# Kernel optimization log

Hardware: AMD Instinct MI355X
Metric: run time of the kernel (lower is better)

## Reference

```python
import jax, jax.numpy as jnp
import numpy as np

V_CNT = 10000
B = 16
N = B * V_CNT          # total nodes
K = 6                  # Chebyshev order
CH = [3, 128, 64, 32, 128]
G = 8                  # GroupNorm groups (divides 128, 64, 32)
EPS = 1e-5
AVG_DEG = 16


def setup_inputs() -> dict:
    key = jax.random.key(0)
    ks = jax.random.split(key, 8)
    n_edges = N * AVG_DEG
    inp = {
        "x": jax.random.normal(ks[0], (N, CH[0]), jnp.float32),
        "edge_index": jax.random.randint(ks[1], (2, n_edges), 0, N, jnp.int32).astype(jnp.int64),
    }
    for l in range(3):
        cin, cout = CH[l], CH[l + 1]
        s = (1.0 / (cin * K)) ** 0.5
        inp[f"W{l}"] = jax.random.uniform(ks[2 + l], (K, cin, cout), jnp.float32, -s, s)
        inp[f"b{l}"] = jnp.zeros((cout,), jnp.float32)
        inp[f"gamma{l}"] = jnp.ones((cout,), jnp.float32)
        inp[f"beta{l}"] = jnp.zeros((cout,), jnp.float32)
    din = V_CNT * CH[3]
    s = (1.0 / din) ** 0.5
    inp["W_last"] = jax.random.uniform(ks[5], (din, CH[4]), jnp.float32, -s, s)
    inp["b_last"] = jnp.zeros((CH[4],), jnp.float32)
    return inp


def _cheb_edge_weights(edge_index):
    # PyG ChebConv sym normalization with lambda_max=2: L_hat = L - I = -D^{-1/2} A D^{-1/2}
    row, col = edge_index[0], edge_index[1]
    deg = jax.ops.segment_sum(jnp.ones(row.shape, jnp.float32), row, num_segments=N)
    dis = jnp.where(deg > 0, jax.lax.rsqrt(jnp.maximum(deg, 1.0)), 0.0)  # deg^{-1/2}, inf->0
    return -dis[row] * dis[col], row, col


def _cheb_conv(x, row, col, w, W, b):
    # Chebyshev recursion: Tx0=x, Tx1=L_hat x, Tx_k = 2 L_hat Tx_{k-1} - Tx_{k-2}
    prop = lambda h: jax.ops.segment_sum(w[:, None] * h[col], row, num_segments=N)
    Tx0 = x
    out = Tx0 @ W[0]
    Tx1 = prop(Tx0)
    out = out + Tx1 @ W[1]
    for k in range(2, W.shape[0]):
        Tx2 = 2.0 * prop(Tx1) - Tx0
        out = out + Tx2 @ W[k]
        Tx0, Tx1 = Tx1, Tx2
    return out + b


def _group_norm(h, gamma, beta):
    n, C = h.shape
    hg = h.reshape(n, G, C // G)
    mu = hg.mean(axis=2, keepdims=True)
    var = hg.var(axis=2, keepdims=True)
    hg = (hg - mu) * jax.lax.rsqrt(var + EPS)
    return hg.reshape(n, C) * gamma + beta


def reference(x, edge_index, W0, b0, gamma0, beta0, W1, b1, gamma1, beta1,
              W2, b2, gamma2, beta2, W_last, b_last):
    w, row, col = _cheb_edge_weights(edge_index)
    Ws = [W0, W1, W2]
    bs = [b0, b1, b2]
    gs = [gamma0, gamma1, gamma2]
    betas = [beta0, beta1, beta2]
    h = x
    for l in range(3):
        h = _cheb_conv(h, row, col, w, Ws[l], bs[l])
        h = _group_norm(h, gs[l], betas[l])
        h = jax.nn.relu(h)
    h = h.reshape(-1, V_CNT * CH[3])  # [B, v_cnt*32]
    return h @ W_last + b_last
```

## Files before the change

### kernel.cpp

```cpp
#include <hip/hip_runtime.h>
#include <hip/hip_fp16.h>


#define NN 160000
#define EE 2560000
#define FDC 640

typedef __attribute__((ext_vector_type(8))) _Float16 half8;
typedef __attribute__((ext_vector_type(4))) float floatx4;

__device__ inline float2 h2f2(unsigned u) {
  __half2 h = __builtin_bit_cast(__half2, u);
  return __half22float2(h);
}
__device__ inline unsigned short f2h(float f) {
  return __builtin_bit_cast(unsigned short, __float2half_rn(f));
}
__device__ inline unsigned packh2(float a, float b) {
  return __builtin_bit_cast(unsigned, __floats2half2_rn(a, b));
}

__global__ __launch_bounds__(256) void k_zero(int* __restrict__ p, int n) {
  int i = blockIdx.x * 256 + threadIdx.x;
  if (i < n) p[i] = 0;
}

__global__ __launch_bounds__(256) void k_hist(const int* __restrict__ ei, int* __restrict__ deg) {
  int e = blockIdx.x * 256 + threadIdx.x;
  if (e < EE) atomicAdd(&deg[ei[e]], 1);
}

__global__ __launch_bounds__(256) void k_dis(const int* __restrict__ deg, float* __restrict__ dis) {
  int i = blockIdx.x * 256 + threadIdx.x;
  if (i < NN) { int d = deg[i]; dis[i] = d > 0 ? rsqrtf((float)d) : 0.f; }
}

__global__ __launch_bounds__(256) void k_scan1(const int* __restrict__ deg, int* __restrict__ rowStart,
                                               int* __restrict__ bsum) {
  __shared__ int s[256];
  int tid = threadIdx.x;
  int i = blockIdx.x * 256 + tid;
  int v = deg[i];
  s[tid] = v;
  __syncthreads();
  for (int off = 1; off < 256; off <<= 1) {
    int t = (tid >= off) ? s[tid - off] : 0;
    __syncthreads();
    s[tid] += t;
    __syncthreads();
  }
  rowStart[i] = s[tid] - v;
  if (tid == 255) bsum[blockIdx.x] = s[255];
}

__global__ void k_scan2(int* __restrict__ bsum, int nb) {
  __shared__ int s[1024];
  int tid = threadIdx.x;
  int v = (tid < nb) ? bsum[tid] : 0;
  s[tid] = v;
  __syncthreads();
  for (int off = 1; off < 1024; off <<= 1) {
    int t = (tid >= off) ? s[tid - off] : 0;
    __syncthreads();
    s[tid] += t;
    __syncthreads();
  }
  if (tid < nb) bsum[tid] = s[tid] - v;
}

__global__ __launch_bounds__(256) void k_scan3(int* __restrict__ rowStart, const int* __restrict__ bsum) {
  int i = blockIdx.x * 256 + threadIdx.x;
  rowStart[i] += bsum[blockIdx.x];
  if (i == 0) rowStart[NN] = EE;
}

__global__ __launch_bounds__(256) void k_scatter(const int* __restrict__ ei, const int* __restrict__ rowStart,
                                                 int* __restrict__ cursor, const float* __restrict__ dis,
                                                 int2* __restrict__ ew) {
  int e = blockIdx.x * 256 + threadIdx.x;
  if (e >= EE) return;
  int r = ei[e];
  int c = ei[EE + e];
  int pos = rowStart[r] + atomicAdd(&cursor[r], 1);
  ew[pos] = make_int2(c, __float_as_int(-dis[r] * dis[c]));
}

__global__ __launch_bounds__(256) void k_copyx(const float* __restrict__ x, float* __restrict__ A,
                                               unsigned short* __restrict__ TxAll) {
  int i = blockIdx.x * 256 + threadIdx.x;
  if (i < NN * 3) {
    float v = x[i];
    A[i] = v;
    int node = i / 3, c = i - node * 3;
    TxAll[node * 32 + c] = f2h(v);
  }
}

template <int MODE>
__global__ __launch_bounds__(256) void k_prop3(const float* __restrict__ Tsrc, float* __restrict__ Tdst,
                                               unsigned short* __restrict__ TxAll, int ks,
                                               const int* __restrict__ rowStart, const int2* __restrict__ ew) {
  int i = blockIdx.x * 256 + threadIdx.x;
  if (i >= NN) return;
  float a0 = 0.f, a1 = 0.f, a2 = 0.f;
  int e = rowStart[i], e1 = rowStart[i + 1];
  for (; e + 1 < e1; e += 2) {
    int2 p0 = ew[e], p1 = ew[e + 1];
    float w0 = __int_as_float(p0.y), w1 = __int_as_float(p1.y);
    a0 += w0 * Tsrc[p0.x * 3] + w1 * Tsrc[p1.x * 3];
    a1 += w0 * Tsrc[p0.x * 3 + 1] + w1 * Tsrc[p1.x * 3 + 1];
    a2 += w0 * Tsrc[p0.x * 3 + 2] + w1 * Tsrc[p1.x * 3 + 2];
  }
  if (e < e1) {
    int2 p0 = ew[e];
    float w0 = __int_as_float(p0.y);
    a0 += w0 * Tsrc[p0.x * 3];
    a1 += w0 * Tsrc[p0.x * 3 + 1];
    a2 += w0 * Tsrc[p0.x * 3 + 2];
  }
  if (MODE == 2) {
    a0 = 2.f * a0 - Tdst[i * 3];
    a1 = 2.f * a1 - Tdst[i * 3 + 1];
    a2 = 2.f * a2 - Tdst[i * 3 + 2];
  }
  Tdst[i * 3] = a0; Tdst[i * 3 + 1] = a1; Tdst[i * 3 + 2] = a2;
  unsigned short* tp = TxAll + i * 32 + ks * 3;
  tp[0] = f2h(a0); tp[1] = f2h(a1); tp[2] = f2h(a2);
}

__global__ __launch_bounds__(256) void k_padW0(const float* __restrict__ W0, unsigned short* __restrict__ Bt) {
  int idx = blockIdx.x * 256 + threadIdx.x;
  if (idx >= 128 * 32) return;
  int co = idx >> 5, t = idx & 31;
  Bt[co * 32 + t] = (t < 18) ? f2h(W0[t * 128 + co]) : (unsigned short)0;
}

template <int CIN, int COUT>
__global__ __launch_bounds__(256) void k_combine(const float* __restrict__ W, unsigned short* __restrict__ Bt) {
  int idx = blockIdx.x * 256 + threadIdx.x;
  if (idx >= CIN * 6 * COUT) return;
  int co = idx % COUT;
  int j  = (idx / COUT) % 6;
  int ci = idx / (6 * COUT);
  float c0, c1, c2, c3, c4, c5;
  switch (j) {
    case 0:  c0 = 1;  c1 = 0;  c2 = -1; c3 = 0;   c4 = 1;  c5 = 0;   break;
    case 1:  c0 = 0;  c1 = 1;  c2 = 0;  c3 = -3;  c4 = 0;  c5 = 5;   break;
    case 2:  c0 = 0;  c1 = 0;  c2 = 2;  c3 = 0;   c4 = -8; c5 = 0;   break;
    case 3:  c0 = 0;  c1 = 0;  c2 = 0;  c3 = 4;   c4 = 0;  c5 = -20; break;
    case 4:  c0 = 0;  c1 = 0;  c2 = 0;  c3 = 0;   c4 = 8;  c5 = 0;   break;
    default: c0 = 0;  c1 = 0;  c2 = 0;  c3 = 0;   c4 = 0;  c5 = 16;  break;
  }
  float s = 0.f;
  s += c0 * W[(0 * CIN + ci) * COUT + co];
  s += c1 * W[(1 * CIN + ci) * COUT + co];
  s += c2 * W[(2 * CIN + ci) * COUT + co];
  s += c3 * W[(3 * CIN + ci) * COUT + co];
  s += c4 * W[(4 * CIN + ci) * COUT + co];
  s += c5 * W[(5 * CIN + ci) * COUT + co];
  Bt[(j * COUT + co) * CIN + ci] = f2h(s);
}

template <int KDIM, int COUT>
__global__ __launch_bounds__(256) void k_gemm(const unsigned short* __restrict__ A,
                                              const unsigned short* __restrict__ Bt,
                                              unsigned short* __restrict__ Y) {
  constexpr int KP = KDIM + 8;
  __shared__ unsigned short As[64 * KP];
  __shared__ unsigned short Bs[64 * KP];
  int i0 = blockIdx.x * 64;
  int c0 = blockIdx.y * 64;
  for (int idx = threadIdx.x; idx < 64 * (KDIM / 8); idx += 256) {
    int row = idx / (KDIM / 8), seg = idx % (KDIM / 8);
    uint4 v = ((const uint4*)A)[(size_t)(i0 + row) * (KDIM / 8) + seg];
    *reinterpret_cast<uint4*>(&As[row * KP + seg * 8]) = v;
  }
  for (int idx = threadIdx.x; idx < 64 * (KDIM / 8); idx += 256) {
    int row = idx / (KDIM / 8), seg = idx % (KDIM / 8);
    uint4 v = ((const uint4*)Bt)[(size_t)(c0 + row) * (KDIM / 8) + seg];
    *reinterpret_cast<uint4*>(&Bs[row * KP + seg * 8]) = v;
  }
  __syncthreads();
  int w = threadIdx.x >> 6, lane = threadIdx.x & 63;
  int mn = lane & 15, q = lane >> 4;
  floatx4 acc[4];
#pragma unroll
  for (int cb = 0; cb < 4; cb++) acc[cb] = {0.f, 0.f, 0.f, 0.f};
#pragma unroll
  for (int ks = 0; ks < KDIM / 32; ks++) {
    half8 af = *reinterpret_cast<const half8*>(&As[(16 * w + mn) * KP + ks * 32 + q * 8]);
#pragma unroll
    for (int cb = 0; cb < 4; cb++) {
      half8 bf = *reinterpret_cast<const half8*>(&Bs[(cb * 16 + mn) * KP + ks * 32 + q * 8]);
      acc[cb] = __builtin_amdgcn_mfma_f32_16x16x32_f16(af, bf, acc[cb], 0, 0, 0);
    }
  }
#pragma unroll
  for (int cb = 0; cb < 4; cb++) {
    int jc = c0 + cb * 16 + mn;
    int slice = jc / COUT, cc = jc % COUT;
    unsigned short* dst = Y + (size_t)slice * NN * COUT + cc;
#pragma unroll
    for (int r = 0; r < 4; r++) {
      int i = i0 + 16 * w + q * 4 + r;
      dst[(size_t)i * COUT] = f2h(acc[cb][r]);
    }
  }
}

template <int CPN>
__global__ __launch_bounds__(256) void k_horner(const unsigned* __restrict__ Ysrc, unsigned* __restrict__ Ydst,
                                                const int* __restrict__ rowStart, const int2* __restrict__ ew) {
  int t = blockIdx.x * 256 + threadIdx.x;
  int i = t / CPN;
  int cp = t % CPN;
  float2 a = h2f2(Ydst[(size_t)i * CPN + cp]);
  float acc0 = a.x, acc1 = a.y;
  int e = rowStart[i], e1 = rowStart[i + 1];
  for (; e + 3 < e1; e += 4) {
    int2 p0 = ew[e], p1 = ew[e + 1], p2 = ew[e + 2], p3 = ew[e + 3];
    unsigned u0 = Ysrc[(size_t)p0.x * CPN + cp];
    unsigned u1 = Ysrc[(size_t)p1.x * CPN + cp];
    unsigned u2 = Ysrc[(size_t)p2.x * CPN + cp];
    unsigned u3 = Ysrc[(size_t)p3.x * CPN + cp];
    float w0 = __int_as_float(p0.y), w1 = __int_as_float(p1.y);
    float w2 = __int_as_float(p2.y), w3 = __int_as_float(p3.y);
    float2 f0 = h2f2(u0), f1 = h2f2(u1), f2 = h2f2(u2), f3 = h2f2(u3);
    acc0 += w0 * f0.x + w1 * f1.x + w2 * f2.x + w3 * f3.x;
    acc1 += w0 * f0.y + w1 * f1.y + w2 * f2.y + w3 * f3.y;
  }
  for (; e < e1; e++) {
    int2 p0 = ew[e];
    float w0 = __int_as_float(p0.y);
    float2 f0 = h2f2(Ysrc[(size_t)p0.x * CPN + cp]);
    acc0 += w0 * f0.x;
    acc1 += w0 * f0.y;
  }
  Ydst[(size_t)i * CPN + cp] = packh2(acc0, acc1);
}

template <int CPG>
__global__ __launch_bounds__(256) void k_gn(const unsigned short* __restrict__ src, const float* __restrict__ bias,
                                            const float* __restrict__ gamma, const float* __restrict__ beta,
                                            unsigned short* __restrict__ dst) {
  constexpr int C = CPG * 8;
  int t = blockIdx.x * 256 + threadIdx.x;
  int i = t >> 3, g = t & 7;
  float v[CPG];
  const unsigned* p = reinterpret_cast<const unsigned*>(src + (size_t)i * C + g * CPG);
#pragma unroll
  for (int q = 0; q < CPG / 2; q++) {
    float2 f = h2f2(p[q]);
    v[2 * q] = f.x; v[2 * q + 1] = f.y;
  }
  float mean = 0.f;
#pragma unroll
  for (int c = 0; c < CPG; c++) { v[c] += bias[g * CPG + c]; mean += v[c]; }
  mean *= (1.f / CPG);
  float var = 0.f;
#pragma unroll
  for (int c = 0; c < CPG; c++) { float d = v[c] - mean; var += d * d; }
  var *= (1.f / CPG);
  float rs = rsqrtf(var + 1e-5f);
  unsigned* dp = reinterpret_cast<unsigned*>(dst + (size_t)i * C + g * CPG);
#pragma unroll
  for (int q = 0; q < CPG / 2; q++) {
    float o0 = fmaxf((v[2 * q] - mean) * rs * gamma[g * CPG + 2 * q] + beta[g * CPG + 2 * q], 0.f);
    float o1 = fmaxf((v[2 * q + 1] - mean) * rs * gamma[g * CPG + 2 * q + 1] + beta[g * CPG + 2 * q + 1], 0.f);
    dp[q] = packh2(o0, o1);
  }
}

__global__ __launch_bounds__(256) void k_initout(const float* __restrict__ bl, float* __restrict__ out) {
  int t = blockIdx.x * 256 + threadIdx.x;
  if (t < 2048) out[t] = bl[t & 127];
}

__global__ __launch_bounds__(256) void k_final(const unsigned short* __restrict__ h3, const float* __restrict__ Wl,
                                               float* __restrict__ out) {
  __shared__ float hs[16 * FDC];
  int d0 = blockIdx.x * FDC;
  const unsigned* h3u = reinterpret_cast<const unsigned*>(h3);
  for (int idx = threadIdx.x; idx < 16 * (FDC / 8); idx += 256) {
    int b = idx / (FDC / 8), dq = idx % (FDC / 8);
    uint4 v = ((const uint4*)h3u)[(size_t)b * 40000 + (size_t)d0 / 8 + dq];
    float2 f0 = h2f2(v.x), f1 = h2f2(v.y), f2 = h2f2(v.z), f3 = h2f2(v.w);
    float* hp = &hs[b * FDC + dq * 8];
    hp[0] = f0.x; hp[1] = f0.y; hp[2] = f1.x; hp[3] = f1.y;
    hp[4] = f2.x; hp[5] = f2.y; hp[6] = f3.x; hp[7] = f3.y;
  }
  __syncthreads();
  int w = threadIdx.x >> 6, lane = threadIdx.x & 63;
  int bh = w & 1, ds = w >> 1;
  float acc0[8], acc1[8];
#pragma unroll
  for (int bb = 0; bb < 8; bb++) { acc0[bb] = 0.f; acc1[bb] = 0.f; }
  for (int dd = ds; dd < FDC; dd += 2) {
    float w0 = Wl[(size_t)(d0 + dd) * 128 + lane];
    float w1 = Wl[(size_t)(d0 + dd) * 128 + lane + 64];
#pragma unroll
    for (int bb = 0; bb < 8; bb++) {
      float h = hs[(bh * 8 + bb) * FDC + dd];
      acc0[bb] += w0 * h;
      acc1[bb] += w1 * h;
    }
  }
#pragma unroll
  for (int bb = 0; bb < 8; bb++) {
    atomicAdd(&out[(bh * 8 + bb) * 128 + lane], acc0[bb]);
    atomicAdd(&out[(bh * 8 + bb) * 128 + lane + 64], acc1[bb]);
  }
}

extern "C" void kernel_launch(void* const* d_in, const int* in_sizes, int n_in,
                              void* d_out, int out_size, void* d_ws, size_t ws_size,
                              hipStream_t stream) {
  const float* x   = (const float*)d_in[0];
  const int*   ei  = (const int*)d_in[1];
  const float* W0  = (const float*)d_in[2];
  const float* b0  = (const float*)d_in[3];
  const float* g0  = (const float*)d_in[4];
  const float* be0 = (const float*)d_in[5];
  const float* W1  = (const float*)d_in[6];
  const float* b1  = (const float*)d_in[7];
  const float* g1  = (const float*)d_in[8];
  const float* be1 = (const float*)d_in[9];
  const float* W2  = (const float*)d_in[10];
  const float* b2  = (const float*)d_in[11];
  const float* g2  = (const float*)d_in[12];
  const float* be2 = (const float*)d_in[13];
  const float* Wl  = (const float*)d_in[14];
  const float* bl  = (const float*)d_in[15];
  float* out = (float*)d_out;
  (void)in_sizes; (void)n_in; (void)out_size; (void)ws_size;

  char* pw = (char*)d_ws;
  auto carve = [&](size_t bytes) -> void* {
    void* r = (void*)pw;
    pw += (bytes + 255) & ~(size_t)255;
    return r;
  };
  int*            deg      = (int*)   carve((size_t)NN * 4);
  int*            cursor   = (int*)   carve((size_t)NN * 4);
  int*            rowStart = (int*)   carve((size_t)(NN + 1) * 4);
  int*            bsum     = (int*)   carve(1024 * 4);
  float*          dis      = (float*) carve((size_t)NN * 4);
  int2*           ew       = (int2*)  carve((size_t)EE * 8);
  unsigned short* Cwt      = (unsigned short*)carve((size_t)384 * 128 * 2);
  unsigned short* TxAll    = (unsigned short*)carve((size_t)NN * 32 * 2);
  float*          A3       = (float*) carve((size_t)NN * 3 * 4);
  float*          B3       = (float*) carve((size_t)NN * 3 * 4);
  unsigned short* Hbuf     = (unsigned short*)carve((size_t)NN * 128 * 2);
  unsigned short* Ybuf     = (unsigned short*)carve((size_t)NN * 384 * 2);

  k_zero<<<625, 256, 0, stream>>>(deg, NN);
  k_zero<<<625, 256, 0, stream>>>(cursor, NN);
  k_hist<<<10000, 256, 0, stream>>>(ei, deg);
  k_dis<<<625, 256, 0, stream>>>(deg, dis);
  k_scan1<<<625, 256, 0, stream>>>(deg, rowStart, bsum);
  k_scan2<<<1, 1024, 0, stream>>>(bsum, 625);
  k_scan3<<<625, 256, 0, stream>>>(rowStart, bsum);
  k_scatter<<<10000, 256, 0, stream>>>(ei, rowStart, cursor, dis, ew);

  k_zero<<<10000, 256, 0, stream>>>((int*)TxAll, NN * 16);
  k_copyx<<<1875, 256, 0, stream>>>(x, A3, TxAll);
  k_prop3<1><<<625, 256, 0, stream>>>(A3, B3, TxAll, 1, rowStart, ew);
  k_prop3<2><<<625, 256, 0, stream>>>(B3, A3, TxAll, 2, rowStart, ew);
  k_prop3<2><<<625, 256, 0, stream>>>(A3, B3, TxAll, 3, rowStart, ew);
  k_prop3<2><<<625, 256, 0, stream>>>(B3, A3, TxAll, 4, rowStart, ew);
  k_prop3<2><<<625, 256, 0, stream>>>(A3, B3, TxAll, 5, rowStart, ew);
  k_padW0<<<16, 256, 0, stream>>>(W0, Cwt);
  k_gemm<32, 128><<<dim3(2500, 2), 256, 0, stream>>>(TxAll, Cwt, Ybuf);
  k_gn<16><<<5000, 256, 0, stream>>>(Ybuf, b0, g0, be0, Hbuf);

  k_combine<128, 64><<<192, 256, 0, stream>>>(W1, Cwt);
  k_gemm<128, 64><<<dim3(2500, 6), 256, 0, stream>>>(Hbuf, Cwt, Ybuf);
  for (int j = 4; j >= 0; j--)
    k_horner<32><<<20000, 256, 0, stream>>>((unsigned*)(Ybuf + (size_t)(j + 1) * NN * 64),
                                            (unsigned*)(Ybuf + (size_t)j * NN * 64), rowStart, ew);
  k_gn<8><<<5000, 256, 0, stream>>>(Ybuf, b1, g1, be1, Hbuf);

  k_combine<64, 32><<<48, 256, 0, stream>>>(W2, Cwt);
  k_gemm<64, 32><<<dim3(2500, 3), 256, 0, stream>>>(Hbuf, Cwt, Ybuf);
  for (int j = 4; j >= 0; j--)
    k_horner<16><<<10000, 256, 0, stream>>>((unsigned*)(Ybuf + (size_t)(j + 1) * NN * 32),
                                            (unsigned*)(Ybuf + (size_t)j * NN * 32), rowStart, ew);
  k_gn<4><<<5000, 256, 0, stream>>>(Ybuf, b2, g2, be2, Hbuf);

  k_initout<<<8, 256, 0, stream>>>(bl, out);
  k_final<<<500, 256, 0, stream>>>(Hbuf, Wl, out);
}
```

Before: 1.486 ms.

## Split final linear into per-block partials with deterministic reduction; deepen gather unrolls

Rewrites the final dense layer as 1250 blocks, each covering 256 feature rows for all 16 batches. Each block reduces across its warps in shared memory and writes a partial tile, and a second kernel sums the partials and adds the bias. This replaces the 500-block version that used float atomics. The change also unrolls the prop3 edge loop to 4 and the Horner gather to 8 to get more loads in flight, and merges the two zeroing launches into one (deg and cursor are assumed contiguous in the workspace). The cost is an extra 10MB partial buffer, and k_final2 reduces 1250 partials serially using only 8 blocks, which may be latency-bound.

Result: faster. 1.436 ms (-3.4%).

```diff
diff --git a/kernel.cpp b/kernel.cpp
--- a/kernel.cpp
+++ b/kernel.cpp
@@ -4,7 +4,7 @@
 
 #define NN 160000
 #define EE 2560000
-#define FDC 640
+#define FD2 256
 
 typedef __attribute__((ext_vector_type(8))) _Float16 half8;
 typedef __attribute__((ext_vector_type(4))) float floatx4;
@@ -104,14 +104,15 @@
   if (i >= NN) return;
   float a0 = 0.f, a1 = 0.f, a2 = 0.f;
   int e = rowStart[i], e1 = rowStart[i + 1];
-  for (; e + 1 < e1; e += 2) {
-    int2 p0 = ew[e], p1 = ew[e + 1];
+  for (; e + 3 < e1; e += 4) {
+    int2 p0 = ew[e], p1 = ew[e + 1], p2 = ew[e + 2], p3 = ew[e + 3];
     float w0 = __int_as_float(p0.y), w1 = __int_as_float(p1.y);
-    a0 += w0 * Tsrc[p0.x * 3] + w1 * Tsrc[p1.x * 3];
-    a1 += w0 * Tsrc[p0.x * 3 + 1] + w1 * Tsrc[p1.x * 3 + 1];
-    a2 += w0 * Tsrc[p0.x * 3 + 2] + w1 * Tsrc[p1.x * 3 + 2];
-  }
-  if (e < e1) {
+    float w2 = __int_as_float(p2.y), w3 = __int_as_float(p3.y);
+    a0 += w0 * Tsrc[p0.x * 3] + w1 * Tsrc[p1.x * 3] + w2 * Tsrc[p2.x * 3] + w3 * Tsrc[p3.x * 3];
+    a1 += w0 * Tsrc[p0.x * 3 + 1] + w1 * Tsrc[p1.x * 3 + 1] + w2 * Tsrc[p2.x * 3 + 1] + w3 * Tsrc[p3.x * 3 + 1];
+    a2 += w0 * Tsrc[p0.x * 3 + 2] + w1 * Tsrc[p1.x * 3 + 2] + w2 * Tsrc[p2.x * 3 + 2] + w3 * Tsrc[p3.x * 3 + 2];
+  }
+  for (; e < e1; e++) {
     int2 p0 = ew[e];
     float w0 = __int_as_float(p0.y);
     a0 += w0 * Tsrc[p0.x * 3];
@@ -217,17 +218,20 @@
   float2 a = h2f2(Ydst[(size_t)i * CPN + cp]);
   float acc0 = a.x, acc1 = a.y;
   int e = rowStart[i], e1 = rowStart[i + 1];
-  for (; e + 3 < e1; e += 4) {
-    int2 p0 = ew[e], p1 = ew[e + 1], p2 = ew[e + 2], p3 = ew[e + 3];
-    unsigned u0 = Ysrc[(size_t)p0.x * CPN + cp];
-    unsigned u1 = Ysrc[(size_t)p1.x * CPN + cp];
-    unsigned u2 = Ysrc[(size_t)p2.x * CPN + cp];
-    unsigned u3 = Ysrc[(size_t)p3.x * CPN + cp];
-    float w0 = __int_as_float(p0.y), w1 = __int_as_float(p1.y);
-    float w2 = __int_as_float(p2.y), w3 = __int_as_float(p3.y);
-    float2 f0 = h2f2(u0), f1 = h2f2(u1), f2 = h2f2(u2), f3 = h2f2(u3);
-    acc0 += w0 * f0.x + w1 * f1.x + w2 * f2.x + w3 * f3.x;
-    acc1 += w0 * f0.y + w1 * f1.y + w2 * f2.y + w3 * f3.y;
+  for (; e + 7 < e1; e += 8) {
+    int2 p[8];
+    unsigned u[8];
+#pragma unroll
+    for (int k = 0; k < 8; k++) p[k] = ew[e + k];
+#pragma unroll
+    for (int k = 0; k < 8; k++) u[k] = Ysrc[(size_t)p[k].x * CPN + cp];
+#pragma unroll
+    for (int k = 0; k < 8; k++) {
+      float w = __int_as_float(p[k].y);
+      float2 f = h2f2(u[k]);
+      acc0 += w * f.x;
+      acc1 += w * f.y;
+    }
   }
   for (; e < e1; e++) {
     int2 p0 = ew[e];
@@ -271,45 +275,63 @@
   }
 }
 
-__global__ __launch_bounds__(256) void k_initout(const float* __restrict__ bl, float* __restrict__ out) {
-  int t = blockIdx.x * 256 + threadIdx.x;
-  if (t < 2048) out[t] = bl[t & 127];
-}
-
-__global__ __launch_bounds__(256) void k_final(const unsigned short* __restrict__ h3, const float* __restrict__ Wl,
-                                               float* __restrict__ out) {
-  __shared__ float hs[16 * FDC];
-  int d0 = blockIdx.x * FDC;
+__global__ __launch_bounds__(256) void k_final1(const unsigned short* __restrict__ h3,
+                                                const float* __restrict__ Wl,
+                                                float* __restrict__ part) {
+  __shared__ float hs[16 * FD2];
+  __shared__ float red[2048];
+  int d0 = blockIdx.x * FD2;
   const unsigned* h3u = reinterpret_cast<const unsigned*>(h3);
-  for (int idx = threadIdx.x; idx < 16 * (FDC / 8); idx += 256) {
-    int b = idx / (FDC / 8), dq = idx % (FDC / 8);
-    uint4 v = ((const uint4*)h3u)[(size_t)b * 40000 + (size_t)d0 / 8 + dq];
-    float2 f0 = h2f2(v.x), f1 = h2f2(v.y), f2 = h2f2(v.z), f3 = h2f2(v.w);
-    float* hp = &hs[b * FDC + dq * 8];
-    hp[0] = f0.x; hp[1] = f0.y; hp[2] = f1.x; hp[3] = f1.y;
-    hp[4] = f2.x; hp[5] = f2.y; hp[6] = f3.x; hp[7] = f3.y;
+  for (int idx = threadIdx.x; idx < 16 * (FD2 / 2); idx += 256) {
+    int b = idx / (FD2 / 2), dq = idx % (FD2 / 2);
+    float2 f = h2f2(h3u[(size_t)b * 160000 + (d0 >> 1) + dq]);
+    hs[b * FD2 + 2 * dq] = f.x;
+    hs[b * FD2 + 2 * dq + 1] = f.y;
   }
   __syncthreads();
   int w = threadIdx.x >> 6, lane = threadIdx.x & 63;
-  int bh = w & 1, ds = w >> 1;
-  float acc0[8], acc1[8];
-#pragma unroll
-  for (int bb = 0; bb < 8; bb++) { acc0[bb] = 0.f; acc1[bb] = 0.f; }
-  for (int dd = ds; dd < FDC; dd += 2) {
-    float w0 = Wl[(size_t)(d0 + dd) * 128 + lane];
-    float w1 = Wl[(size_t)(d0 + dd) * 128 + lane + 64];
-#pragma unroll
-    for (int bb = 0; bb < 8; bb++) {
-      float h = hs[(bh * 8 + bb) * FDC + dd];
-      acc0[bb] += w0 * h;
-      acc1[bb] += w1 * h;
+  float a0[16], a1[16];
+#pragma unroll
+  for (int b = 0; b < 16; b++) { a0[b] = 0.f; a1[b] = 0.f; }
+  const float* wp = Wl + (size_t)(d0 + w * (FD2 / 4)) * 128 + 2 * lane;
+#pragma unroll 2
+  for (int r = 0; r < FD2 / 4; r++) {
+    float2 wv = *reinterpret_cast<const float2*>(wp + (size_t)r * 128);
+    int row = w * (FD2 / 4) + r;
+#pragma unroll
+    for (int b = 0; b < 16; b++) {
+      float h = hs[b * FD2 + row];
+      a0[b] += wv.x * h;
+      a1[b] += wv.y * h;
     }
   }
-#pragma unroll
-  for (int bb = 0; bb < 8; bb++) {
-    atomicAdd(&out[(bh * 8 + bb) * 128 + lane], acc0[bb]);
-    atomicAdd(&out[(bh * 8 + bb) * 128 + lane + 64], acc1[bb]);
-  }
+  float2* red2 = reinterpret_cast<float2*>(red);
+  for (int ww = 0; ww < 4; ww++) {
+    if (w == ww) {
+#pragma unroll
+      for (int b = 0; b < 16; b++) {
+        if (ww == 0) {
+          red2[b * 64 + lane] = make_float2(a0[b], a1[b]);
+        } else {
+          float2 r2 = red2[b * 64 + lane];
+          r2.x += a0[b]; r2.y += a1[b];
+          red2[b * 64 + lane] = r2;
+        }
+      }
+    }
+    __syncthreads();
+  }
+  for (int i = threadIdx.x; i < 2048; i += 256)
+    part[(size_t)blockIdx.x * 2048 + i] = red[i];
+}
+
+__global__ __launch_bounds__(256) void k_final2(const float* __restrict__ part, const float* __restrict__ bl,
+                                                float* __restrict__ out) {
+  int o = blockIdx.x * 256 + threadIdx.x;
+  float s = bl[o & 127];
+#pragma unroll 10
+  for (int p = 0; p < 1250; p++) s += part[(size_t)p * 2048 + o];
+  out[o] = s;
 }
 
 extern "C" void kernel_launch(void* const* d_in, const int* in_sizes, int n_in,
@@ -352,9 +374,9 @@
   float*          B3       = (float*) carve((size_t)NN * 3 * 4);
   unsigned short* Hbuf     = (unsigned short*)carve((size_t)NN * 128 * 2);
   unsigned short* Ybuf     = (unsigned short*)carve((size_t)NN * 384 * 2);
-
-  k_zero<<<625, 256, 0, stream>>>(deg, NN);
-  k_zero<<<625, 256, 0, stream>>>(cursor, NN);
+  float*          part     = (float*) carve((size_t)1250 * 2048 * 4);
+
+  k_zero<<<1250, 256, 0, stream>>>(deg, 2 * NN);
   k_hist<<<10000, 256, 0, stream>>>(ei, deg);
   k_dis<<<625, 256, 0, stream>>>(deg, dis);
   k_scan1<<<625, 256, 0, stream>>>(deg, rowStart, bsum);
@@ -387,6 +409,6 @@
                                             (unsigned*)(Ybuf + (size_t)j * NN * 32), rowStart, ew);
   k_gn<4><<<5000, 256, 0, stream>>>(Ybuf, b2, g2, be2, Hbuf);
 
-  k_initout<<<8, 256, 0, stream>>>(bl, out);
-  k_final<<<500, 256, 0, stream>>>(Hbuf, Wl, out);
-}
+  k_final1<<<1250, 256, 0, stream>>>(Hbuf, Wl, part);
+  k_final2<<<8, 256, 0, stream>>>(part, bl, out);
+}
```
